# Kernel optimization log

Hardware: AMD Instinct MI355X
Metric: run time of the kernel (lower is better)

Reference implementation:

```python
import jax, jax.numpy as jnp
import numpy as np

N = 100000
E = 640000
WIDTH = 128
NUM_FEATURES = 64


def _linear_relu(h, W, b):
    # LinearBlock with batch_norm=False, dropout=0.0 -> Linear + ReLU
    return jax.nn.relu(h @ W + b)


def setup_inputs() -> dict:
    key = jax.random.key(0)
    k = jax.random.split(key, 8)
    x = jax.random.normal(k[0], (N, WIDTH), dtype=jnp.float32)
    e = jax.random.randint(k[1], (2, E), 0, N, dtype=jnp.int32)
    e_feat = jax.random.normal(k[2], (E, NUM_FEATURES), dtype=jnp.float32)
    s_e = 1.0 / np.sqrt(WIDTH + NUM_FEATURES)
    s_m = 1.0 / np.sqrt(2 * WIDTH)
    W_edge = jax.random.uniform(k[3], (WIDTH + NUM_FEATURES, WIDTH), jnp.float32, -s_e, s_e)
    b_edge = jax.random.uniform(k[4], (WIDTH,), jnp.float32, -s_e, s_e)
    W_mlp = jax.random.uniform(k[5], (2 * WIDTH, WIDTH), jnp.float32, -s_m, s_m)
    b_mlp = jax.random.uniform(k[6], (WIDTH,), jnp.float32, -s_m, s_m)
    return {"x": x, "e": e, "e_feat": e_feat, "W_edge": W_edge, "b_edge": b_edge,
            "W_mlp": W_mlp, "b_mlp": b_mlp}


def reference(x, e, e_feat, W_edge, b_edge, W_mlp, b_mlp):
    src, dst = e[0], e[1]
    diffs = x[dst] - x[src]                                   # [E, width]
    ef = diffs + _linear_relu(jnp.concatenate([diffs, e_feat], axis=1), W_edge, b_edge)
    maxes = jax.ops.segment_max(ef, dst, num_segments=x.shape[0])  # [N, width]
    # torch_scatter.scatter_max leaves empty segments at 0
    maxes = jnp.where(jnp.isneginf(maxes), 0.0, maxes)
    return x + _linear_relu(jnp.concatenate([x, maxes], axis=1), W_mlp, b_mlp)
```

## Files before the change

### kernel.cpp

```cpp
#include <hip/hip_runtime.h>
#include <hip/hip_bf16.h>
#include <limits.h>

#define NNODES 100000
#define NEDGES 640000
#define WIDTH  128
#define NFEAT  64
#define KA     192
#define KA_PAD 196
#define KB     256
#define KB_PAD 264
#define MT     64
#define STC    68
#define NB_SCAN ((NNODES + 255) / 256)
#define NB_HIST ((NEDGES + 255) / 256)
#define NB_PREP (((KA + KB) * WIDTH + 255) / 256)

typedef __attribute__((ext_vector_type(8))) short short8;
typedef __attribute__((ext_vector_type(4))) short short4v;
typedef __attribute__((ext_vector_type(4))) float floatx4;

__device__ __forceinline__ short f2bf_rne(float f) {
    unsigned u = __float_as_uint(f);
    unsigned r = u + 0x7fffu + ((u >> 16) & 1u);
    return (short)(r >> 16);
}
__device__ __forceinline__ short f2bf_t(float f) {
    return (short)(__float_as_uint(f) >> 16);
}
__device__ __forceinline__ float bf2f(short s) {
    return __uint_as_float(((unsigned)(unsigned short)s) << 16);
}
__device__ __forceinline__ unsigned encu(float f) {
    unsigned u = __float_as_uint(f);
    return (u & 0x80000000u) ? ~u : (u | 0x80000000u);
}
__device__ __forceinline__ float decu(unsigned e) {
    unsigned u = (e & 0x80000000u) ? (e ^ 0x80000000u) : ~e;
    return __uint_as_float(u);
}

__global__ __launch_bounds__(256) void prep_hist_kernel(
    const int* __restrict__ e, int* __restrict__ counts,
    const float* __restrict__ W_edge, const float* __restrict__ W_mlp,
    short* __restrict__ We_t, short* __restrict__ Wm_t)
{
    int b = blockIdx.x;
    if (b < NB_HIST) {
        int i = b * 256 + threadIdx.x;
        if (i < NEDGES) atomicAdd(&counts[e[NEDGES + i]], 1);
    } else {
        int t = (b - NB_HIST) * 256 + threadIdx.x;
        if (t < KA * WIDTH) {
            int k = t / WIDTH, n = t % WIDTH;
            We_t[n * KA + k] = f2bf_rne(W_edge[t]);
        } else if (t < (KA + KB) * WIDTH) {
            int j = t - KA * WIDTH;
            int k = j / WIDTH, n = j % WIDTH;
            Wm_t[n * KB + k] = f2bf_rne(W_mlp[j]);
        }
    }
}

__global__ __launch_bounds__(256) void scanA_kernel(
    const int* __restrict__ counts, int* __restrict__ cursor, int* __restrict__ blockSum)
{
    __shared__ int s[256];
    int tid = threadIdx.x;
    int n = blockIdx.x * 256 + tid;
    int c = (n < NNODES) ? counts[n] : 0;
    s[tid] = c;
    __syncthreads();
    for (int off = 1; off < 256; off <<= 1) {
        int v = (tid >= off) ? s[tid - off] : 0;
        __syncthreads();
        s[tid] += v;
        __syncthreads();
    }
    if (n < NNODES) cursor[n] = s[tid] - c;
    if (tid == 255) blockSum[blockIdx.x] = s[255];
}

__global__ __launch_bounds__(512) void scanB_kernel(int* __restrict__ blockSum,
                                                    int* __restrict__ blockOff)
{
    __shared__ int s[512];
    int tid = threadIdx.x;
    int c = (tid < NB_SCAN) ? blockSum[tid] : 0;
    s[tid] = c;
    __syncthreads();
    for (int off = 1; off < 512; off <<= 1) {
        int v = (tid >= off) ? s[tid - off] : 0;
        __syncthreads();
        s[tid] += v;
        __syncthreads();
    }
    if (tid < NB_SCAN) blockOff[tid] = s[tid] - c;
}

__global__ __launch_bounds__(256) void scatter_kernel(
    const int* __restrict__ e, int* __restrict__ cursor,
    const int* __restrict__ blockOff,
    uint2* __restrict__ pSD, int* __restrict__ pEid)
{
    int i = blockIdx.x * 256 + threadIdx.x;
    if (i < NEDGES) {
        int s = e[i];
        int d = e[NEDGES + i];
        int p = atomicAdd(&cursor[d], 1) + blockOff[d >> 8];
        pSD[p] = make_uint2((unsigned)s, (unsigned)d);
        pEid[p] = i;
    }
}

__global__ __launch_bounds__(256, 6) void edge_kernel(
    const float* __restrict__ x, const float* __restrict__ e_feat,
    const short* __restrict__ We_t, const float* __restrict__ b_edge,
    const uint2* __restrict__ pSD, const int* __restrict__ pEid,
    unsigned* __restrict__ mEnc)
{
    __shared__ __align__(16) short sA[MT * KA_PAD];
    __shared__ float sBias[WIDTH];
    __shared__ int   sDst[MT];
    __shared__ int   sHeadRow[MT + 1];
    __shared__ int   sMeta[3];

    const int tid = threadIdx.x;
    if (tid < WIDTH) sBias[tid] = b_edge[tid];

    const int bid = blockIdx.x;
    const int btile = (bid & 7) * (NEDGES / MT / 8) + (bid >> 3);
    const int e0 = btile * MT;

    const float4* xf4 = (const float4*)x;
    const float4* ef4 = (const float4*)e_feat;

    {
        int mq = tid >> 5, c = tid & 31;
        uint2 sd[8];
        #pragma unroll
        for (int j = 0; j < 8; ++j) sd[j] = pSD[e0 + mq + 8 * j];
        int mq2 = tid >> 4, c2 = tid & 15;
        int eid[4];
        #pragma unroll
        for (int j = 0; j < 4; ++j) eid[j] = pEid[e0 + mq2 + 16 * j];

        float4 xsA[4], xdA[4];
        #pragma unroll
        for (int j = 0; j < 4; ++j) {
            xsA[j] = xf4[(size_t)sd[j].x * 32 + c];
            xdA[j] = xf4[(size_t)sd[j].y * 32 + c];
        }
        float4 xsB[4], xdB[4];
        #pragma unroll
        for (int j = 0; j < 4; ++j) {
            xsB[j] = xf4[(size_t)sd[4 + j].x * 32 + c];
            xdB[j] = xf4[(size_t)sd[4 + j].y * 32 + c];
        }
        if (c == 0) {
            #pragma unroll
            for (int j = 0; j < 8; ++j) sDst[mq + 8 * j] = (int)sd[j].y;
        }
        #pragma unroll
        for (int j = 0; j < 4; ++j) {
            int mm = mq + 8 * j;
            short4v df;
            df.x = f2bf_t(xdA[j].x - xsA[j].x);
            df.y = f2bf_t(xdA[j].y - xsA[j].y);
            df.z = f2bf_t(xdA[j].z - xsA[j].z);
            df.w = f2bf_t(xdA[j].w - xsA[j].w);
            *(short4v*)&sA[mm * KA_PAD + c * 4] = df;
        }
        float4 fv[4];
        #pragma unroll
        for (int j = 0; j < 4; ++j) fv[j] = ef4[(size_t)eid[j] * 16 + c2];
        #pragma unroll
        for (int j = 0; j < 4; ++j) {
            int mm = mq + 8 * (4 + j);
            short4v df;
            df.x = f2bf_t(xdB[j].x - xsB[j].x);
            df.y = f2bf_t(xdB[j].y - xsB[j].y);
            df.z = f2bf_t(xdB[j].z - xsB[j].z);
            df.w = f2bf_t(xdB[j].w - xsB[j].w);
            *(short4v*)&sA[mm * KA_PAD + c * 4] = df;
        }
        #pragma unroll
        for (int j = 0; j < 4; ++j) {
            int mm = mq2 + 16 * j;
            short4v sv;
            sv.x = f2bf_t(fv[j].x); sv.y = f2bf_t(fv[j].y);
            sv.z = f2bf_t(fv[j].z); sv.w = f2bf_t(fv[j].w);
            *(short4v*)&sA[mm * KA_PAD + WIDTH + c2 * 4] = sv;
        }
    }
    __syncthreads();

    if (tid < 64) {
        bool head = (tid == 0) || (sDst[tid] != sDst[tid - 1]);
        unsigned long long mask = __ballot(head);
        int rank = __popcll(mask & ((1ull << tid) - 1ull));
        if (head) sHeadRow[rank] = tid;
        if (tid == 0) {
            int nh = (int)__popcll(mask);
            sMeta[0] = nh;
            sHeadRow[nh] = MT;
            int prevSame = 0, nextSame = 0;
            if (e0 > 0)           prevSame = (pSD[e0 - 1].y  == (unsigned)sDst[0]);
            if (e0 + MT < NEDGES) nextSame = (pSD[e0 + MT].y == (unsigned)sDst[MT - 1]);
            sMeta[1] = prevSame; sMeta[2] = nextSame;
        }
    }

    const int wave = tid >> 6;
    const int lane = tid & 63;
    const int l15  = lane & 15;
    const int kq   = (lane >> 4) << 3;
    const int quad = lane >> 4;

    floatx4 acc[4][2];
    #pragma unroll
    for (int rt = 0; rt < 4; ++rt)
        #pragma unroll
        for (int ct = 0; ct < 2; ++ct)
            acc[rt][ct] = (floatx4){0.f, 0.f, 0.f, 0.f};

    #pragma unroll
    for (int kc = 0; kc < 6; ++kc) {
        int k0 = kc * 32 + kq;
        short8 a[4];
        #pragma unroll
        for (int rt = 0; rt < 4; ++rt)
            a[rt] = *(const short8*)&sA[(rt * 16 + l15) * KA_PAD + k0];
        short8 b[2];
        #pragma unroll
        for (int ct = 0; ct < 2; ++ct)
            b[ct] = *(const short8*)&We_t[(size_t)(wave * 32 + ct * 16 + l15) * KA + k0];
        #pragma unroll
        for (int rt = 0; rt < 4; ++rt)
            #pragma unroll
            for (int ct = 0; ct < 2; ++ct)
                acc[rt][ct] = __builtin_amdgcn_mfma_f32_16x16x32_bf16(a[rt], b[ct], acc[rt][ct], 0, 0, 0);
    }

    #pragma unroll
    for (int rt = 0; rt < 4; ++rt) {
        #pragma unroll
        for (int ct = 0; ct < 2; ++ct) {
            int col = wave * 32 + ct * 16 + l15;
            float bias = sBias[col];
            #pragma unroll
            for (int i = 0; i < 4; ++i) {
                int row = rt * 16 + quad * 4 + i;
                float v = acc[rt][ct][i] + bias;
                v = v > 0.f ? v : 0.f;
                acc[rt][ct][i] = v + bf2f(sA[row * KA_PAD + col]);
            }
        }
    }
    __syncthreads();

    short* sT = sA;
    #pragma unroll
    for (int rt = 0; rt < 4; ++rt) {
        #pragma unroll
        for (int ct = 0; ct < 2; ++ct) {
            int col = wave * 32 + ct * 16 + l15;
            short4v pk;
            pk.x = f2bf_t(acc[rt][ct][0]);
            pk.y = f2bf_t(acc[rt][ct][1]);
            pk.z = f2bf_t(acc[rt][ct][2]);
            pk.w = f2bf_t(acc[rt][ct][3]);
            *(short4v*)&sT[col * STC + rt * 16 + quad * 4] = pk;
        }
    }
    __syncthreads();

    const int nh = sMeta[0], prevSame = sMeta[1], nextSame = sMeta[2];
    const unsigned* sT32 = (const unsigned*)sT;
    for (int p = tid; p < (nh << 7); p += 256) {
        int h = p >> 7, c = p & 127;
        int r0 = sHeadRow[h], r1 = sHeadRow[h + 1];
        const unsigned* colp = sT32 + c * (STC / 2);
        int w0 = r0 >> 1, w1 = (r1 - 1) >> 1;
        float m = -3.4e38f;
        for (int w = w0; w <= w1; ++w) {
            unsigned u = colp[w];
            float flo = bf2f((short)(u & 0xffffu));
            float fhi = bf2f((short)(u >> 16));
            if (2 * w >= r0)    m = fmaxf(m, flo);
            if (2 * w + 1 < r1) m = fmaxf(m, fhi);
        }
        int dst = sDst[r0];
        unsigned ev = encu(m);
        unsigned* dp = &mEnc[(size_t)dst * WIDTH + c];
        bool atom = (h == 0 && prevSame) || (h == nh - 1 && nextSame);
        if (atom) atomicMax(dp, ev);
        else      *dp = ev;
    }
}

__global__ __launch_bounds__(256) void node_kernel(
    const float* __restrict__ x, const short* __restrict__ Wm_t,
    const float* __restrict__ b_mlp, float* __restrict__ out)
{
    __shared__ short sA[MT * KB_PAD];
    __shared__ float sBias[WIDTH];

    const int tid = threadIdx.x;
    if (tid < WIDTH) sBias[tid] = b_mlp[tid];

    const int n0 = blockIdx.x * MT;
    const float4* xf4 = (const float4*)x;
    const uint4* enc4 = (const uint4*)out;

    {
        int mq = tid >> 5, c = tid & 31;
        #pragma unroll
        for (int mm = mq; mm < MT; mm += 8) {
            int node = n0 + mm;
            if (node >= NNODES) node = NNODES - 1;
            float4 xv = xf4[(size_t)node * 32 + c];
            short4v sx;
            sx.x = f2bf_rne(xv.x); sx.y = f2bf_rne(xv.y);
            sx.z = f2bf_rne(xv.z); sx.w = f2bf_rne(xv.w);
            *(short4v*)&sA[mm * KB_PAD + c * 4] = sx;
            uint4 ev = enc4[(size_t)node * 32 + c];
            short4v sm;
            sm.x = f2bf_rne(ev.x == 0u ? 0.f : decu(ev.x));
            sm.y = f2bf_rne(ev.y == 0u ? 0.f : decu(ev.y));
            sm.z = f2bf_rne(ev.z == 0u ? 0.f : decu(ev.z));
            sm.w = f2bf_rne(ev.w == 0u ? 0.f : decu(ev.w));
            *(short4v*)&sA[mm * KB_PAD + WIDTH + c * 4] = sm;
        }
    }
    __syncthreads();

    const int wave = tid >> 6;
    const int lane = tid & 63;
    const int l15  = lane & 15;
    const int kq   = (lane >> 4) << 3;
    const int quad = lane >> 4;

    floatx4 acc[4][2];
    #pragma unroll
    for (int rt = 0; rt < 4; ++rt)
        #pragma unroll
        for (int ct = 0; ct < 2; ++ct)
            acc[rt][ct] = (floatx4){0.f, 0.f, 0.f, 0.f};

    #pragma unroll
    for (int kc = 0; kc < 8; ++kc) {
        int k0 = kc * 32 + kq;
        short8 a[4];
        #pragma unroll
        for (int rt = 0; rt < 4; ++rt)
            a[rt] = *(const short8*)&sA[(rt * 16 + l15) * KB_PAD + k0];
        short8 b[2];
        #pragma unroll
        for (int ct = 0; ct < 2; ++ct)
            b[ct] = *(const short8*)&Wm_t[(size_t)(wave * 32 + ct * 16 + l15) * KB + k0];
        #pragma unroll
        for (int rt = 0; rt < 4; ++rt)
            #pragma unroll
            for (int ct = 0; ct < 2; ++ct)
                acc[rt][ct] = __builtin_amdgcn_mfma_f32_16x16x32_bf16(a[rt], b[ct], acc[rt][ct], 0, 0, 0);
    }

    #pragma unroll
    for (int rt = 0; rt < 4; ++rt) {
        #pragma unroll
        for (int ct = 0; ct < 2; ++ct) {
            int col = wave * 32 + ct * 16 + l15;
            float bias = sBias[col];
            #pragma unroll
            for (int i = 0; i < 4; ++i) {
                int row = rt * 16 + quad * 4 + i;
                int node = n0 + row;
                if (node < NNODES) {
                    float v = acc[rt][ct][i] + bias;
                    v = v > 0.f ? v : 0.f;
                    out[(size_t)node * WIDTH + col] = x[(size_t)node * WIDTH + col] + v;
                }
            }
        }
    }
}

extern "C" void kernel_launch(void* const* d_in, const int* in_sizes, int n_in,
                              void* d_out, int out_size, void* d_ws, size_t ws_size,
                              hipStream_t stream) {
    const float* x      = (const float*)d_in[0];
    const int*   e      = (const int*)d_in[1];
    const float* e_feat = (const float*)d_in[2];
    const float* W_edge = (const float*)d_in[3];
    const float* b_edge = (const float*)d_in[4];
    const float* W_mlp  = (const float*)d_in[5];
    const float* b_mlp  = (const float*)d_in[6];
    float*    out  = (float*)d_out;
    unsigned* mEnc = (unsigned*)d_out;

    short* We_t = (short*)d_ws;
    short* Wm_t = We_t + (size_t)KA * WIDTH;
    int* base     = (int*)((char*)d_ws + 114688);
    uint2* pSD    = (uint2*)base;
    int* pEid     = (int*)(base + 2 * NEDGES);
    int* counts   = pEid + NEDGES;
    int* cursor   = counts + NNODES;
    int* blockSum = cursor + NNODES;
    int* blockOff = blockSum + NB_SCAN;

    hipMemsetAsync(d_out, 0, (size_t)NNODES * WIDTH * 4, stream);
    hipMemsetAsync(counts, 0, (size_t)NNODES * 4, stream);
    prep_hist_kernel<<<NB_HIST + NB_PREP, 256, 0, stream>>>(e, counts, W_edge, W_mlp, We_t, Wm_t);
    scanA_kernel<<<NB_SCAN, 256, 0, stream>>>(counts, cursor, blockSum);
    scanB_kernel<<<1, 512, 0, stream>>>(blockSum, blockOff);
    scatter_kernel<<<(NEDGES + 255) / 256, 256, 0, stream>>>(e, cursor, blockOff, pSD, pEid);
    edge_kernel<<<NEDGES / MT, 256, 0, stream>>>(x, e_feat, We_t, b_edge, pSD, pEid, mEnc);
    node_kernel<<<(NNODES + MT - 1) / MT, 256, 0, stream>>>(x, Wm_t, b_mlp, out);
}
```

Baseline: 536.2 us.

## Simplify edge gather loop, drop tile swizzle, relax launch bounds

Replaces the manually batched x gathers, where all loads were issued before the conversions, with a simple per-row load-convert-store loop. It also removes the XCD-style block-to-tile swizzle, lowers the occupancy hint from 6 to 4 blocks per CU and widens the LDS row pad from 196 to 200. Together these change register pressure, memory-level parallelism, bank-conflict patterns and cache locality across dies. Fewer loads in flight per thread may expose more gather latency, though the compiler may still hoist loads across the unrolled loop.

```diff
diff --git a/kernel.cpp b/kernel.cpp
--- a/kernel.cpp
+++ b/kernel.cpp
@@ -7,7 +7,7 @@
 #define WIDTH  128
 #define NFEAT  64
 #define KA     192
-#define KA_PAD 196
+#define KA_PAD 200
 #define KB     256
 #define KB_PAD 264
 #define MT     64
@@ -113,7 +113,7 @@
     }
 }
 
-__global__ __launch_bounds__(256, 6) void edge_kernel(
+__global__ __launch_bounds__(256, 4) void edge_kernel(
     const float* __restrict__ x, const float* __restrict__ e_feat,
     const short* __restrict__ We_t, const float* __restrict__ b_edge,
     const uint2* __restrict__ pSD, const int* __restrict__ pEid,
@@ -128,10 +128,7 @@
     const int tid = threadIdx.x;
     if (tid < WIDTH) sBias[tid] = b_edge[tid];
 
-    const int bid = blockIdx.x;
-    const int btile = (bid & 7) * (NEDGES / MT / 8) + (bid >> 3);
-    const int e0 = btile * MT;
-
+    const int e0 = blockIdx.x * MT;
     const float4* xf4 = (const float4*)x;
     const float4* ef4 = (const float4*)e_feat;
 
@@ -140,56 +137,30 @@
         uint2 sd[8];
         #pragma unroll
         for (int j = 0; j < 8; ++j) sd[j] = pSD[e0 + mq + 8 * j];
+        #pragma unroll
+        for (int j = 0; j < 8; ++j) {
+            int mm = mq + 8 * j;
+            float4 xs = xf4[(size_t)sd[j].x * 32 + c];
+            float4 xd = xf4[(size_t)sd[j].y * 32 + c];
+            short4v df;
+            df.x = f2bf_t(xd.x - xs.x);
+            df.y = f2bf_t(xd.y - xs.y);
+            df.z = f2bf_t(xd.z - xs.z);
+            df.w = f2bf_t(xd.w - xs.w);
+            *(short4v*)&sA[mm * KA_PAD + c * 4] = df;
+            if (c == 0) sDst[mm] = (int)sd[j].y;
+        }
         int mq2 = tid >> 4, c2 = tid & 15;
         int eid[4];
         #pragma unroll
         for (int j = 0; j < 4; ++j) eid[j] = pEid[e0 + mq2 + 16 * j];
-
-        float4 xsA[4], xdA[4];
-        #pragma unroll
-        for (int j = 0; j < 4; ++j) {
-            xsA[j] = xf4[(size_t)sd[j].x * 32 + c];
-            xdA[j] = xf4[(size_t)sd[j].y * 32 + c];
-        }
-        float4 xsB[4], xdB[4];
-        #pragma unroll
-        for (int j = 0; j < 4; ++j) {
-            xsB[j] = xf4[(size_t)sd[4 + j].x * 32 + c];
-            xdB[j] = xf4[(size_t)sd[4 + j].y * 32 + c];
-        }
-        if (c == 0) {
-            #pragma unroll
-            for (int j = 0; j < 8; ++j) sDst[mq + 8 * j] = (int)sd[j].y;
-        }
-        #pragma unroll
-        for (int j = 0; j < 4; ++j) {
-            int mm = mq + 8 * j;
-            short4v df;
-            df.x = f2bf_t(xdA[j].x - xsA[j].x);
-            df.y = f2bf_t(xdA[j].y - xsA[j].y);
-            df.z = f2bf_t(xdA[j].z - xsA[j].z);
-            df.w = f2bf_t(xdA[j].w - xsA[j].w);
-            *(short4v*)&sA[mm * KA_PAD + c * 4] = df;
-        }
-        float4 fv[4];
-        #pragma unroll
-        for (int j = 0; j < 4; ++j) fv[j] = ef4[(size_t)eid[j] * 16 + c2];
-        #pragma unroll
-        for (int j = 0; j < 4; ++j) {
-            int mm = mq + 8 * (4 + j);
-            short4v df;
-            df.x = f2bf_t(xdB[j].x - xsB[j].x);
-            df.y = f2bf_t(xdB[j].y - xsB[j].y);
-            df.z = f2bf_t(xdB[j].z - xsB[j].z);
-            df.w = f2bf_t(xdB[j].w - xsB[j].w);
-            *(short4v*)&sA[mm * KA_PAD + c * 4] = df;
-        }
         #pragma unroll
         for (int j = 0; j < 4; ++j) {
             int mm = mq2 + 16 * j;
+            float4 fv = ef4[(size_t)eid[j] * 16 + c2];
             short4v sv;
-            sv.x = f2bf_t(fv[j].x); sv.y = f2bf_t(fv[j].y);
-            sv.z = f2bf_t(fv[j].z); sv.w = f2bf_t(fv[j].w);
+            sv.x = f2bf_t(fv.x); sv.y = f2bf_t(fv.y);
+            sv.z = f2bf_t(fv.z); sv.w = f2bf_t(fv.w);
             *(short4v*)&sA[mm * KA_PAD + WIDTH + c2 * 4] = sv;
         }
     }
```

New measurement: 493.7 us. -7.9%, faster.
